# Kernel optimization log

Measured on AMD Instinct MI355X. Metric: run time of the kernel, lower is better.

The kernel has to match this reference:

```python
import jax, jax.numpy as jnp
import numpy as np

B, T, C = 2, 2048, 1024
H = 16
D = C // H
STRIDE = 2
EPS = 1e-5


def _strided_allowed(T, stride):
    # position i attends to j if j<=i and (j >= i-4 local band OR j % stride == 0)
    i = jnp.arange(T)[:, None]
    j = jnp.arange(T)[None, :]
    return (j <= i) & ((j >= i - 4) | (j % stride == 0))


def _layernorm(x, w, b):
    mu = jnp.mean(x, axis=-1, keepdims=True)
    var = jnp.mean(jnp.square(x - mu), axis=-1, keepdims=True)
    return (x - mu) * jax.lax.rsqrt(var + EPS) * w + b


def setup_inputs() -> dict:
    key = jax.random.key(0)
    ks = jax.random.split(key, 8)
    s = 0.02
    return {
        "x": jax.random.normal(ks[0], (B, T, C), dtype=jnp.float32),
        "ln1_w": jnp.ones((C,), jnp.float32),
        "ln1_b": jnp.zeros((C,), jnp.float32),
        "c_attn_w": s * jax.random.normal(ks[1], (C, 3 * C), jnp.float32),  # [in,out]
        "c_attn_b": jnp.zeros((3 * C,), jnp.float32),
        "attn_proj_w": s * jax.random.normal(ks[2], (C, C), jnp.float32),
        "attn_proj_b": jnp.zeros((C,), jnp.float32),
        "ln2_w": jnp.ones((C,), jnp.float32),
        "ln2_b": jnp.zeros((C,), jnp.float32),
        "fc_w": s * jax.random.normal(ks[3], (C, 4 * C), jnp.float32),
        "fc_b": jnp.zeros((4 * C,), jnp.float32),
        "mlp_proj_w": s * jax.random.normal(ks[4], (4 * C, C), jnp.float32),
        "mlp_proj_b": jnp.zeros((C,), jnp.float32),
    }


def reference(x, ln1_w, ln1_b, c_attn_w, c_attn_b, attn_proj_w, attn_proj_b,
              ln2_w, ln2_b, fc_w, fc_b, mlp_proj_w, mlp_proj_b):
    Bx, Tx, Cx = x.shape
    # --- sparse (strided) causal attention on ln_1(x) ---
    h = _layernorm(x, ln1_w, ln1_b)
    qkv = h @ c_attn_w + c_attn_b                      # [B,T,3C]
    q, k, v = jnp.split(qkv, 3, axis=-1)
    q = q.reshape(Bx, Tx, H, D).transpose(0, 2, 1, 3)  # [B,H,T,D]
    k = k.reshape(Bx, Tx, H, D).transpose(0, 2, 1, 3)
    v = v.reshape(Bx, Tx, H, D).transpose(0, 2, 1, 3)
    scale = 1.0 / np.sqrt(D)
    att = jnp.einsum('bhqd,bhkd->bhqk', q, k) * scale  # dense [B,H,T,T] as in source
    allowed = _strided_allowed(Tx, STRIDE)             # [T,T] bool
    att = jnp.where(allowed[None, None], att, -jnp.inf)
    att = jax.nn.softmax(att, axis=-1)
    y = jnp.einsum('bhqk,bhkd->bhqd', att, v)
    y = y.transpose(0, 2, 1, 3).reshape(Bx, Tx, Cx)
    y = y @ attn_proj_w + attn_proj_b
    x = x + y
    # --- MLP on ln_2(x) ---
    h2 = _layernorm(x, ln2_w, ln2_b)
    h2 = jax.nn.gelu(h2 @ fc_w + fc_b, approximate=False)
    x = x + (h2 @ mlp_proj_w + mlp_proj_b)
    return x
```

## Files before the change

### kernel.cpp

```cpp
#include <hip/hip_runtime.h>
#include <hip/hip_bf16.h>

#define Bn 2
#define Tn 2048
#define Cn 1024
#define Hn 16
#define Dn 64
#define Mrows (Bn * Tn)

typedef __attribute__((ext_vector_type(8))) short short8;
typedef __attribute__((ext_vector_type(4))) float f32x4;

typedef const __attribute__((address_space(1))) unsigned int* gas_ptr;
typedef __attribute__((address_space(3))) unsigned int* las_ptr;

__device__ __forceinline__ unsigned short f2b(float f) {
  unsigned int u = __builtin_bit_cast(unsigned int, f);
  return (unsigned short)((u + 0x7fffu + ((u >> 16) & 1u)) >> 16);
}

__device__ __forceinline__ float gelu_f(float v) {
  float u2 = v + 0.044715f * v * v * v;
  float e = __expf(1.5957691216f * u2);
  float th = 1.0f - 2.0f / (e + 1.0f);
  return 0.5f * v * (1.0f + th);
}

__device__ __forceinline__ void ln_row(const float* __restrict__ x, const float* __restrict__ w,
                                       const float* __restrict__ b, unsigned short* __restrict__ out,
                                       int row, float* ls, float* ls2) {
  const int t = threadIdx.x;
  const float4 v = *reinterpret_cast<const float4*>(x + (size_t)row * Cn + t * 4);
  float s = v.x + v.y + v.z + v.w;
  float s2 = v.x * v.x + v.y * v.y + v.z * v.z + v.w * v.w;
#pragma unroll
  for (int m = 1; m < 64; m <<= 1) { s += __shfl_xor(s, m); s2 += __shfl_xor(s2, m); }
  if ((t & 63) == 0) { ls[t >> 6] = s; ls2[t >> 6] = s2; }
  __syncthreads();
  s  = ls[0] + ls[1] + ls[2] + ls[3];
  s2 = ls2[0] + ls2[1] + ls2[2] + ls2[3];
  const float mu = s * (1.0f / Cn);
  const float rstd = rsqrtf(s2 * (1.0f / Cn) - mu * mu + 1e-5f);
  const float4 wv = *reinterpret_cast<const float4*>(w + t * 4);
  const float4 bv = *reinterpret_cast<const float4*>(b + t * 4);
  unsigned short o[4];
  o[0] = f2b((v.x - mu) * rstd * wv.x + bv.x);
  o[1] = f2b((v.y - mu) * rstd * wv.y + bv.y);
  o[2] = f2b((v.z - mu) * rstd * wv.z + bv.z);
  o[3] = f2b((v.w - mu) * rstd * wv.w + bv.w);
  *reinterpret_cast<uint2*>(out + (size_t)row * Cn + t * 4) = *reinterpret_cast<uint2*>(o);
}

__global__ __launch_bounds__(256) void ln_kernel(const float* __restrict__ x,
                                                 const float* __restrict__ w,
                                                 const float* __restrict__ b,
                                                 unsigned short* __restrict__ out) {
  __shared__ float ls[4], ls2[4];
  ln_row(x, w, b, out, blockIdx.x, ls, ls2);
}

__global__ __launch_bounds__(256) void prep_kernel(
    const float* __restrict__ W0, unsigned short* __restrict__ T0,
    const float* __restrict__ W1, unsigned short* __restrict__ T1,
    const float* __restrict__ W2, unsigned short* __restrict__ T2,
    const float* __restrict__ W3, unsigned short* __restrict__ T3,
    const float* __restrict__ x, const float* __restrict__ ln1w,
    const float* __restrict__ ln1b, unsigned short* __restrict__ h) {
  __shared__ float tile[32][33];
  __shared__ float ls[4], ls2[4];
  int b = blockIdx.x;
  if (b >= 12288) {
    ln_row(x, ln1w, ln1b, h, b - 12288, ls, ls2);
    return;
  }
  const float* W; unsigned short* T; int K, N;
  if (b < 3072)      { W = W0; T = T0; K = 1024; N = 3072; }
  else if (b < 4096) { W = W1; T = T1; K = 1024; N = 1024; b -= 3072; }
  else if (b < 8192) { W = W2; T = T2; K = 1024; N = 4096; b -= 4096; }
  else               { W = W3; T = T3; K = 4096; N = 1024; b -= 8192; }
  const int nx = N >> 5;
  const int n0 = (b % nx) * 32, k0 = (b / nx) * 32;
  const int tx = threadIdx.x & 31, ty = threadIdx.x >> 5;
#pragma unroll
  for (int r = 0; r < 4; r++)
    tile[ty + r * 8][tx] = W[(size_t)(k0 + ty + r * 8) * N + n0 + tx];
  __syncthreads();
#pragma unroll
  for (int r = 0; r < 4; r++)
    T[(size_t)(n0 + ty + r * 8) * K + k0 + tx] = f2b(tile[tx][ty + r * 8]);
}

#define BUFS 16384
template <int EP>
__global__ __launch_bounds__(512, 2) void gemm256_kernel(
    const unsigned short* __restrict__ A, const unsigned short* __restrict__ Bt,
    const float* __restrict__ bias, void* out, int M, int N, int K, int nx) {
  extern __shared__ unsigned short lds[];
  const int tid = threadIdx.x;
  const int lane = tid & 63, w = tid >> 6;
  const int wm = w >> 2, wn = w & 3;
  const int l15 = lane & 15, l4 = lane >> 4;

  const int nwg = gridDim.x;
  int wg = blockIdx.x;
  wg = (wg & 7) * (nwg >> 3) + (wg >> 3);
  const int tile_m = (wg / nx) * 256;
  const int tile_n = (wg % nx) * 256;

  f32x4 acc[8][4] = {};

  const int ch0 = w * 64 + lane;
  const int r0 = ch0 >> 2;
  const int c0 = (((ch0 & 3) ^ ((r0 >> 1) & 3))) * 8;
  const unsigned short* gA0 = A + (size_t)(tile_m + r0) * K + c0;
  const unsigned short* gA1 = gA0 + (size_t)128 * K;
  const unsigned short* gB0 = Bt + (size_t)(tile_n + r0) * K + c0;
  const unsigned short* gB1 = gB0 + (size_t)128 * K;
  const int ldsA0 = (w * 64) * 8, ldsA1 = (512 + w * 64) * 8;

  auto stage = [&](unsigned short* Ab, int t) {
    unsigned short* Bb = Ab + 8192;
    const size_t ko = (size_t)t * 32;
    __builtin_amdgcn_global_load_lds((gas_ptr)(gA0 + ko), (las_ptr)&Ab[ldsA0], 16, 0, 0);
    __builtin_amdgcn_global_load_lds((gas_ptr)(gA1 + ko), (las_ptr)&Ab[ldsA1], 16, 0, 0);
    __builtin_amdgcn_global_load_lds((gas_ptr)(gB0 + ko), (las_ptr)&Bb[ldsA0], 16, 0, 0);
    __builtin_amdgcn_global_load_lds((gas_ptr)(gB1 + ko), (las_ptr)&Bb[ldsA1], 16, 0, 0);
  };

  stage(lds, 0);
  stage(lds + BUFS, 1);
  stage(lds + 2 * BUFS, 2);
  asm volatile("s_waitcnt vmcnt(8)" ::: "memory");
  __builtin_amdgcn_s_barrier();
  __builtin_amdgcn_sched_barrier(0);

  const int ca = (l4 ^ ((l15 >> 1) & 3)) * 8;

  const int nt = K >> 5;
  for (int tb = 0; tb < nt; tb += 4) {
#pragma unroll
    for (int u = 0; u < 4; u++) {
      const int t = tb + u;
      if (t + 3 < nt) stage(lds + (((u + 3) & 3) * BUFS), t + 3);

      const unsigned short* Ab = lds + u * BUFS;
      const unsigned short* Bb = Ab + 8192;
      short8 a[4], b[4], a2[4];
#pragma unroll
      for (int i = 0; i < 4; i++) {
        a[i] = *reinterpret_cast<const short8*>(&Ab[(wm * 128 + i * 16 + l15) * 32 + ca]);
        b[i] = *reinterpret_cast<const short8*>(&Bb[(wn * 64 + i * 16 + l15) * 32 + ca]);
      }
      __builtin_amdgcn_sched_barrier(0);
#pragma unroll
      for (int i = 0; i < 4; i++)
        a2[i] = *reinterpret_cast<const short8*>(&Ab[(wm * 128 + 64 + i * 16 + l15) * 32 + ca]);

      asm volatile("s_waitcnt lgkmcnt(4)" ::: "memory");
      __builtin_amdgcn_sched_barrier(0);
      __builtin_amdgcn_s_setprio(1);
#pragma unroll
      for (int mi = 0; mi < 4; mi++)
#pragma unroll
        for (int ni = 0; ni < 4; ni++)
          acc[mi][ni] = __builtin_amdgcn_mfma_f32_16x16x32_bf16(a[mi], b[ni], acc[mi][ni], 0, 0, 0);
      __builtin_amdgcn_s_setprio(0);
      __builtin_amdgcn_sched_barrier(0);

      asm volatile("s_waitcnt lgkmcnt(0)" ::: "memory");
      __builtin_amdgcn_sched_barrier(0);
      __builtin_amdgcn_s_setprio(1);
#pragma unroll
      for (int mi = 0; mi < 4; mi++)
#pragma unroll
        for (int ni = 0; ni < 4; ni++)
          acc[mi + 4][ni] = __builtin_amdgcn_mfma_f32_16x16x32_bf16(a2[mi], b[ni], acc[mi + 4][ni], 0, 0, 0);
      __builtin_amdgcn_s_setprio(0);
      __builtin_amdgcn_sched_barrier(0);

      if (t + 3 < nt) {
        asm volatile("s_waitcnt vmcnt(8)" ::: "memory");
      } else if (t + 2 < nt) {
        asm volatile("s_waitcnt vmcnt(4)" ::: "memory");
      } else if (t + 1 < nt) {
        asm volatile("s_waitcnt vmcnt(0)" ::: "memory");
      }
      __builtin_amdgcn_s_barrier();
      __builtin_amdgcn_sched_barrier(0);
    }
  }

#pragma unroll
  for (int ni = 0; ni < 4; ni++) {
    const int col = tile_n + wn * 64 + ni * 16 + l15;
    const float bv = bias[col];
#pragma unroll
    for (int mi = 0; mi < 8; mi++) {
#pragma unroll
      for (int r = 0; r < 4; r++) {
        const int row = tile_m + wm * 128 + mi * 16 + l4 * 4 + r;
        const size_t idx = (size_t)row * N + col;
        float v = acc[mi][ni][r] + bv;
        if (EP == 0) {
          ((unsigned short*)out)[idx] = f2b(v);
        } else {
          ((unsigned short*)out)[idx] = f2b(gelu_f(v));
        }
      }
    }
  }
}

__global__ __launch_bounds__(512, 1) void gemm128_kernel(
    const unsigned short* __restrict__ A, const unsigned short* __restrict__ Bt,
    const float* __restrict__ bias, const float* __restrict__ res, float* __restrict__ out,
    int M, int N, int K, int nx) {
  extern __shared__ unsigned short lds[];
  const int tid = threadIdx.x;
  const int lane = tid & 63, w = tid >> 6;
  const int wm = w >> 2, wn = w & 3;
  const int l15 = lane & 15, l4 = lane >> 4;

  const int nwg = gridDim.x;
  int wg = blockIdx.x;
  wg = (wg & 7) * (nwg >> 3) + (wg >> 3);
  const int tile_m = (wg / nx) * 128;
  const int tile_n = (wg % nx) * 128;

  f32x4 acc[4][2] = {};

  const unsigned short* Gs = (w < 4) ? A : Bt;
  const int tb0 = (w < 4) ? tile_m : tile_n;
  const int ch0 = (w & 3) * 128 + lane;
  const int r0c = ch0 >> 2;
  const int c0s = (((ch0 & 3) ^ ((r0c >> 1) & 3))) * 8;
  const unsigned short* g0 = Gs + (size_t)(tb0 + r0c) * K + c0s;
  const unsigned short* g1 = g0 + (size_t)16 * K;
  const int lds0 = ((w & 3) * 128) * 8, lds1 = ((w & 3) * 128 + 64) * 8;
  const int half = (w < 4) ? 0 : 4096;

  auto stage = [&](int slot, int t) {
    unsigned short* Lb = lds + slot * 8192 + half;
    const size_t ko = (size_t)t * 32;
    __builtin_amdgcn_global_load_lds((gas_ptr)(g0 + ko), (las_ptr)&Lb[lds0], 16, 0, 0);
    __builtin_amdgcn_global_load_lds((gas_ptr)(g1 + ko), (las_ptr)&Lb[lds1], 16, 0, 0);
  };

  stage(0, 0);
  stage(1, 1);
  stage(2, 2);
  stage(3, 3);
  asm volatile("s_waitcnt vmcnt(4)" ::: "memory");
  __builtin_amdgcn_s_barrier();
  __builtin_amdgcn_sched_barrier(0);

  const int ca = (l4 ^ ((l15 >> 1) & 3)) * 8;

  const int nt = K >> 5;
  const int np = nt >> 1;
  for (int p = 0; p < np; ++p) {
    const int t0 = 2 * p;
    if (t0 + 4 < nt) stage((t0 + 4) % 6, t0 + 4);
    if (t0 + 5 < nt) stage((t0 + 5) % 6, t0 + 5);

    const unsigned short* A0 = lds + (t0 % 6) * 8192;
    const unsigned short* B0 = A0 + 4096;
    const unsigned short* A1 = lds + ((t0 + 1) % 6) * 8192;
    const unsigned short* B1 = A1 + 4096;
    short8 a[2], b[2], a2[2], c[2], d[2], c2[2];
#pragma unroll
    for (int i = 0; i < 2; i++) {
      a[i] = *reinterpret_cast<const short8*>(&A0[(wm * 64 + i * 16 + l15) * 32 + ca]);
      b[i] = *reinterpret_cast<const short8*>(&B0[(wn * 32 + i * 16 + l15) * 32 + ca]);
    }
    __builtin_amdgcn_sched_barrier(0);
#pragma unroll
    for (int i = 0; i < 2; i++)
      a2[i] = *reinterpret_cast<const short8*>(&A0[(wm * 64 + 32 + i * 16 + l15) * 32 + ca]);
    __builtin_amdgcn_sched_barrier(0);
#pragma unroll
    for (int i = 0; i < 2; i++) {
      c[i] = *reinterpret_cast<const short8*>(&A1[(wm * 64 + i * 16 + l15) * 32 + ca]);
      d[i] = *reinterpret_cast<const short8*>(&B1[(wn * 32 + i * 16 + l15) * 32 + ca]);
    }
    __builtin_amdgcn_sched_barrier(0);
#pragma unroll
    for (int i = 0; i < 2; i++)
      c2[i] = *reinterpret_cast<const short8*>(&A1[(wm * 64 + 32 + i * 16 + l15) * 32 + ca]);

    asm volatile("s_waitcnt lgkmcnt(8)" ::: "memory");
    __builtin_amdgcn_sched_barrier(0);
    __builtin_amdgcn_s_setprio(1);
#pragma unroll
    for (int mi = 0; mi < 2; mi++)
#pragma unroll
      for (int ni = 0; ni < 2; ni++)
        acc[mi][ni] = __builtin_amdgcn_mfma_f32_16x16x32_bf16(a[mi], b[ni], acc[mi][ni], 0, 0, 0);
    __builtin_amdgcn_s_setprio(0);
    __builtin_amdgcn_sched_barrier(0);

    asm volatile("s_waitcnt lgkmcnt(6)" ::: "memory");
    __builtin_amdgcn_sched_barrier(0);
    __builtin_amdgcn_s_setprio(1);
#pragma unroll
    for (int mi = 0; mi < 2; mi++)
#pragma unroll
      for (int ni = 0; ni < 2; ni++)
        acc[mi + 2][ni] = __builtin_amdgcn_mfma_f32_16x16x32_bf16(a2[mi], b[ni], acc[mi + 2][ni], 0, 0, 0);
    __builtin_amdgcn_s_setprio(0);
    __builtin_amdgcn_sched_barrier(0);

    asm volatile("s_waitcnt lgkmcnt(2)" ::: "memory");
    __builtin_amdgcn_sched_barrier(0);
    __builtin_amdgcn_s_setprio(1);
#pragma unroll
    for (int mi = 0; mi < 2; mi++)
#pragma unroll
      for (int ni = 0; ni < 2; ni++)
        acc[mi][ni] = __builtin_amdgcn_mfma_f32_16x16x32_bf16(c[mi], d[ni], acc[mi][ni], 0, 0, 0);
    __builtin_amdgcn_s_setprio(0);
    __builtin_amdgcn_sched_barrier(0);

    asm volatile("s_waitcnt lgkmcnt(0)" ::: "memory");
    __builtin_amdgcn_sched_barrier(0);
    __builtin_amdgcn_s_setprio(1);
#pragma unroll
    for (int mi = 0; mi < 2; mi++)
#pragma unroll
      for (int ni = 0; ni < 2; ni++)
        acc[mi + 2][ni] = __builtin_amdgcn_mfma_f32_16x16x32_bf16(c2[mi], d[ni], acc[mi + 2][ni], 0, 0, 0);
    __builtin_amdgcn_s_setprio(0);
    __builtin_amdgcn_sched_barrier(0);

    if (t0 + 4 < nt) {
      asm volatile("s_waitcnt vmcnt(4)" ::: "memory");
    } else if (t0 + 2 < nt) {
      asm volatile("s_waitcnt vmcnt(0)" ::: "memory");
    }
    __builtin_amdgcn_s_barrier();
    __builtin_amdgcn_sched_barrier(0);
  }

#pragma unroll
  for (int ni = 0; ni < 2; ni++) {
    const int col = tile_n + wn * 32 + ni * 16 + l15;
    const float bv = bias[col];
#pragma unroll
    for (int mi = 0; mi < 4; mi++) {
#pragma unroll
      for (int r = 0; r < 4; r++) {
        const int row = tile_m + wm * 64 + mi * 16 + l4 * 4 + r;
        const size_t idx = (size_t)row * N + col;
        out[idx] = acc[mi][ni][r] + bv + res[idx];
      }
    }
  }
}

__global__ __launch_bounds__(256, 4) void attn_kernel(const unsigned short* __restrict__ qkv,
                                                      unsigned short* __restrict__ y) {
  __shared__ unsigned short SH[17408];
  const int tid = threadIdx.x;
  const int lane = tid & 63, w = tid >> 6;
  const int l15 = lane & 15, l4 = lane >> 4;

  const int bi = blockIdx.x;
  const int quarter = bi >> 8, rest = bi & 255;
  const int bh = rest >> 3, sub = rest & 7;
  int qt;
  if (quarter == 0) qt = sub;
  else if (quarter == 1) qt = 15 - sub;
  else if (quarter == 2) qt = 16 + sub;
  else qt = 31 - sub;
  const int bb = bh >> 4, hh = bh & 15;
  const int q0 = qt * 64;
  const size_t base = (size_t)bb * Tn * (3 * Cn) + hh * 64;

  const int nfar = qt >> 1;
  const int ntiles = nfar + (q0 ? 2 : 1);

  unsigned short* Vt = SH + 8192;
  unsigned short* Ps = SH + 12800 + w * 1152;

  auto keyof = [&](int t, int row) -> int {
    if (t < nfar) return t * 128 + 2 * row;
    return q0 - 64 * (ntiles - 1 - t) + row;
  };
  auto stageK = [&](int t) {
    unsigned short* kb = SH + ((t & 1) << 12);
#pragma unroll
    for (int u = 0; u < 2; u++) {
      const int chunk = u * 256 + tid;
      const int row = chunk >> 3, cc = chunk & 7;
      const int csrc = cc ^ (row & 7);
      const int key = keyof(t, row);
      __builtin_amdgcn_global_load_lds(
          (gas_ptr)&qkv[base + Cn + (size_t)key * (3 * Cn) + csrc * 8],
          (las_ptr)&kb[(u * 256 + (w << 6)) * 8], 16, 0, 0);
    }
  };
  uint4 vr[2];
  auto fetchV = [&](int t) {
#pragma unroll
    for (int u = 0; u < 2; u++) {
      const int chunk = u * 256 + tid;
      const int row = chunk >> 3, cc = chunk & 7;
      const int key = keyof(t, row);
      vr[u] = *reinterpret_cast<const uint4*>(&qkv[base + 2 * Cn + (size_t)key * (3 * Cn) + cc * 8]);
    }
  };

#pragma unroll
  for (int u = 0; u < 2; u++) {
    const int chunk = u * 256 + tid;
    const int row = chunk >> 3, cc = chunk & 7;
    const int csrc = cc ^ (row & 7);
    __builtin_amdgcn_global_load_lds(
        (gas_ptr)&qkv[base + (size_t)(q0 + row) * (3 * Cn) + csrc * 8],
        (las_ptr)&SH[(u * 256 + (w << 6)) * 8], 16, 0, 0);
  }
  __syncthreads();
  short8 qf[2];
#pragma unroll
  for (int ks = 0; ks < 2; ks++) {
    const int r = (w << 4) + l15;
    qf[ks] = *reinterpret_cast<const short8*>(&SH[r * 64 + (((ks * 4 + l4) ^ (l15 & 7)) * 8)]);
  }
  asm volatile("s_waitcnt lgkmcnt(0)" ::: "memory");
  __builtin_amdgcn_s_barrier();
  __builtin_amdgcn_sched_barrier(0);
  stageK(0);
  fetchV(0);
  __syncthreads();

  f32x4 acc_o[4] = {};
  float mrow[4], lrow[4];
#pragma unroll
  for (int r = 0; r < 4; r++) { mrow[r] = -1e30f; lrow[r] = 0.0f; }

  for (int t = 0; t < ntiles; ++t) {
#pragma unroll
    for (int u = 0; u < 2; u++) {
      const int chunk = u * 256 + tid;
      const int row = chunk >> 3, cc = chunk & 7;
      unsigned short tmp[8];
      *reinterpret_cast<uint4*>(tmp) = vr[u];
      const int xr = row ^ (cc << 3);
#pragma unroll
      for (int j = 0; j < 8; j++) Vt[(cc * 8 + j) * 72 + xr] = tmp[j];
    }
    if (t + 1 < ntiles) { stageK(t + 1); fetchV(t + 1); }
    asm volatile("s_waitcnt lgkmcnt(0)" ::: "memory");
    __builtin_amdgcn_s_barrier();
    __builtin_amdgcn_sched_barrier(0);

    const unsigned short* Kb = SH + ((t & 1) << 12);
    f32x4 s[4] = {};
#pragma unroll
    for (int ni = 0; ni < 4; ni++) {
#pragma unroll
      for (int ks = 0; ks < 2; ks++) {
        const int r = ni * 16 + l15;
        short8 kf = *reinterpret_cast<const short8*>(&Kb[r * 64 + (((ks * 4 + l4) ^ (l15 & 7)) * 8)]);
        s[ni] = __builtin_amdgcn_mfma_f32_16x16x32_bf16(qf[ks], kf, s[ni], 0, 0, 0);
      }
    }

    const bool far = (t < nfar);
    const int kb0 = far ? t * 128 : q0 - 64 * (ntiles - 1 - t);
#pragma unroll
    for (int ni = 0; ni < 4; ni++) {
      const int pos = ni * 16 + l15;
      const int j = far ? kb0 + 2 * pos : kb0 + pos;
#pragma unroll
      for (int r = 0; r < 4; r++) {
        float v = s[ni][r] * 0.125f;
        if (far) {
          v = (j < q0 - 64) ? v : -1e30f;
        } else {
          const int iq = q0 + (w << 4) + l4 * 4 + r;
          const bool ok = (j <= iq) && ((j >= iq - 4) || ((j & 1) == 0));
          v = ok ? v : -1e30f;
        }
        s[ni][r] = v;
      }
    }

    float tmx[4];
    bool need = false;
#pragma unroll
    for (int r = 0; r < 4; r++) {
      float tm = fmaxf(fmaxf(s[0][r], s[1][r]), fmaxf(s[2][r], s[3][r]));
      tm = fmaxf(tm, __shfl_xor(tm, 1));
      tm = fmaxf(tm, __shfl_xor(tm, 2));
      tm = fmaxf(tm, __shfl_xor(tm, 4));
      tm = fmaxf(tm, __shfl_xor(tm, 8));
      tmx[r] = tm;
      need = need || (tm > mrow[r] + 8.0f);
    }
    if (__any(need)) {
#pragma unroll
      for (int r = 0; r < 4; r++) {
        const float mnew = fmaxf(mrow[r], tmx[r]);
        const float alpha = __expf(mrow[r] - mnew);
        mrow[r] = mnew;
        lrow[r] *= alpha;
#pragma unroll
        for (int nd = 0; nd < 4; nd++) acc_o[nd][r] *= alpha;
      }
    }
#pragma unroll
    for (int r = 0; r < 4; r++) {
      float rs = 0.0f;
#pragma unroll
      for (int ni = 0; ni < 4; ni++) {
        const float pv = __expf(s[ni][r] - mrow[r]);
        s[ni][r] = pv;
        rs += pv;
      }
      rs += __shfl_xor(rs, 1); rs += __shfl_xor(rs, 2);
      rs += __shfl_xor(rs, 4); rs += __shfl_xor(rs, 8);
      lrow[r] += rs;
    }

#pragma unroll
    for (int ni = 0; ni < 4; ni++)
#pragma unroll
      for (int r = 0; r < 4; r++)
        Ps[(l4 * 4 + r) * 72 + ni * 16 + l15] = f2b(s[ni][r]);

#pragma unroll
    for (int kss = 0; kss < 2; kss++) {
      short8 pf = *reinterpret_cast<const short8*>(&Ps[l15 * 72 + kss * 32 + l4 * 8]);
#pragma unroll
      for (int nd = 0; nd < 4; nd++) {
        const int d = nd * 16 + l15;
        const int kcol = (kss * 32 + l4 * 8) ^ ((d >> 3) << 3);
        short8 vf = *reinterpret_cast<const short8*>(&Vt[d * 72 + kcol]);
        acc_o[nd] = __builtin_amdgcn_mfma_f32_16x16x32_bf16(pf, vf, acc_o[nd], 0, 0, 0);
      }
    }

    __syncthreads();
  }

#pragma unroll
  for (int r = 0; r < 4; r++) {
    const float inv = 1.0f / lrow[r];
    const int row = q0 + (w << 4) + l4 * 4 + r;
#pragma unroll
    for (int nd = 0; nd < 4; nd++) {
      const int col = nd * 16 + l15;
      y[((size_t)bb * Tn + row) * Cn + hh * 64 + col] = f2b(acc_o[nd][r] * inv);
    }
  }
}

extern "C" void kernel_launch(void* const* d_in, const int* in_sizes, int n_in,
                              void* d_out, int out_size, void* d_ws, size_t ws_size,
                              hipStream_t stream) {
  const float* x           = (const float*)d_in[0];
  const float* ln1_w       = (const float*)d_in[1];
  const float* ln1_b       = (const float*)d_in[2];
  const float* c_attn_w    = (const float*)d_in[3];
  const float* c_attn_b    = (const float*)d_in[4];
  const float* attn_proj_w = (const float*)d_in[5];
  const float* attn_proj_b = (const float*)d_in[6];
  const float* ln2_w       = (const float*)d_in[7];
  const float* ln2_b       = (const float*)d_in[8];
  const float* fc_w        = (const float*)d_in[9];
  const float* fc_b        = (const float*)d_in[10];
  const float* mlp_proj_w  = (const float*)d_in[11];
  const float* mlp_proj_b  = (const float*)d_in[12];
  float* out = (float*)d_out;

  char* ws = (char*)d_ws;
  unsigned short* wT1 = (unsigned short*)(ws);
  unsigned short* wT2 = (unsigned short*)(ws + 6291456);
  unsigned short* wT3 = (unsigned short*)(ws + 8388608);
  unsigned short* wT4 = (unsigned short*)(ws + 16777216);
  unsigned short* h   = (unsigned short*)(ws + 25165824);
  unsigned short* qkv = (unsigned short*)(ws + 33554432);
  unsigned short* yb  = (unsigned short*)(ws + 67108864);

  hipFuncSetAttribute((const void*)gemm256_kernel<0>, hipFuncAttributeMaxDynamicSharedMemorySize, 131072);
  hipFuncSetAttribute((const void*)gemm256_kernel<2>, hipFuncAttributeMaxDynamicSharedMemorySize, 131072);
  hipFuncSetAttribute((const void*)gemm128_kernel, hipFuncAttributeMaxDynamicSharedMemorySize, 98304);

  prep_kernel<<<16384, 256, 0, stream>>>(c_attn_w, wT1, attn_proj_w, wT2,
                                         fc_w, wT3, mlp_proj_w, wT4,
                                         x, ln1_w, ln1_b, h);
  gemm256_kernel<0><<<(Mrows / 256) * (3072 / 256), 512, 131072, stream>>>(
      h, wT1, c_attn_b, qkv, Mrows, 3072, 1024, 3072 / 256);
  attn_kernel<<<1024, 256, 0, stream>>>(qkv, yb);
  gemm128_kernel<<<(Mrows / 128) * (1024 / 128), 512, 98304, stream>>>(
      yb, wT2, attn_proj_b, x, out, Mrows, 1024, 1024, 1024 / 128);
  ln_kernel<<<Mrows, 256, 0, stream>>>(out, ln2_w, ln2_b, h);
  gemm256_kernel<2><<<(Mrows / 256) * (4096 / 256), 512, 131072, stream>>>(
      h, wT3, fc_b, qkv, Mrows, 4096, 1024, 4096 / 256);
  gemm128_kernel<<<(Mrows / 128) * (1024 / 128), 512, 98304, stream>>>(
      qkv, wT4, mlp_proj_b, out, out, Mrows, 1024, 4096, 1024 / 128);
}
```

Baseline: 221.4 us.

## Retile QKV GEMM to 256x192, use 128-tile GEMM for FC, pipeline attention loads

The QKV projection GEMM moves from 256x256 to 256x192 tiles, with A and B loads split across waves, so the 3072-wide output produces 256 workgroups instead of 192 and fills the CUs better. The FC GEMM switches to the 128x128 kernel, which gains a GELU bf16 epilogue, giving more workgroups. The attention kernel reorders its V/K prefetch and replaces full syncthreads with partial vmcnt waits so global loads overlap compute. The risks are lower per-tile data reuse, lower occupancy from launch_bounds(512,1), and wait counts that must match exactly.

```diff
diff --git a/kernel.cpp b/kernel.cpp
--- a/kernel.cpp
+++ b/kernel.cpp
@@ -90,9 +90,8 @@
     T[(size_t)(n0 + ty + r * 8) * K + k0 + tx] = f2b(tile[tx][ty + r * 8]);
 }
 
-#define BUFS 16384
 template <int EP>
-__global__ __launch_bounds__(512, 2) void gemm256_kernel(
+__global__ __launch_bounds__(512, 1) void gemm192_kernel(
     const unsigned short* __restrict__ A, const unsigned short* __restrict__ Bt,
     const float* __restrict__ bias, void* out, int M, int N, int K, int nx) {
   extern __shared__ unsigned short lds[];
@@ -105,32 +104,36 @@
   int wg = blockIdx.x;
   wg = (wg & 7) * (nwg >> 3) + (wg >> 3);
   const int tile_m = (wg / nx) * 256;
-  const int tile_n = (wg % nx) * 256;
-
-  f32x4 acc[8][4] = {};
-
-  const int ch0 = w * 64 + lane;
+  const int tile_n = (wg % nx) * 192;
+
+  f32x4 acc[8][3] = {};
+
+  const bool isA = (w < 4);
+  const int wl = w & 3;
+  const int ch0 = wl * 64 + lane;
   const int r0 = ch0 >> 2;
   const int c0 = (((ch0 & 3) ^ ((r0 >> 1) & 3))) * 8;
-  const unsigned short* gA0 = A + (size_t)(tile_m + r0) * K + c0;
-  const unsigned short* gA1 = gA0 + (size_t)128 * K;
-  const unsigned short* gB0 = Bt + (size_t)(tile_n + r0) * K + c0;
-  const unsigned short* gB1 = gB0 + (size_t)128 * K;
-  const int ldsA0 = (w * 64) * 8, ldsA1 = (512 + w * 64) * 8;
-
-  auto stage = [&](unsigned short* Ab, int t) {
-    unsigned short* Bb = Ab + 8192;
+  const unsigned short* G = isA ? A : Bt;
+  const int tb0 = isA ? tile_m : tile_n;
+  const unsigned short* g0 = G + (size_t)(tb0 + r0) * K + c0;
+  const int lb = wl * 512;
+
+  auto stage = [&](int slot, int t) {
+    unsigned short* L = lds + slot * 14336 + (isA ? 0 : 8192);
     const size_t ko = (size_t)t * 32;
-    __builtin_amdgcn_global_load_lds((gas_ptr)(gA0 + ko), (las_ptr)&Ab[ldsA0], 16, 0, 0);
-    __builtin_amdgcn_global_load_lds((gas_ptr)(gA1 + ko), (las_ptr)&Ab[ldsA1], 16, 0, 0);
-    __builtin_amdgcn_global_load_lds((gas_ptr)(gB0 + ko), (las_ptr)&Bb[ldsA0], 16, 0, 0);
-    __builtin_amdgcn_global_load_lds((gas_ptr)(gB1 + ko), (las_ptr)&Bb[ldsA1], 16, 0, 0);
+#pragma unroll
+    for (int j = 0; j < 4; j++) {
+      if (isA || j < 3)
+        __builtin_amdgcn_global_load_lds((gas_ptr)(g0 + (size_t)64 * K * j + ko),
+                                         (las_ptr)&L[lb + j * 2048], 16, 0, 0);
+    }
   };
 
-  stage(lds, 0);
-  stage(lds + BUFS, 1);
-  stage(lds + 2 * BUFS, 2);
-  asm volatile("s_waitcnt vmcnt(8)" ::: "memory");
+  stage(0, 0);
+  stage(1, 1);
+  stage(2, 2);
+  if (isA) asm volatile("s_waitcnt vmcnt(8)" ::: "memory");
+  else     asm volatile("s_waitcnt vmcnt(6)" ::: "memory");
   __builtin_amdgcn_s_barrier();
   __builtin_amdgcn_sched_barrier(0);
 
@@ -141,16 +144,17 @@
 #pragma unroll
     for (int u = 0; u < 4; u++) {
       const int t = tb + u;
-      if (t + 3 < nt) stage(lds + (((u + 3) & 3) * BUFS), t + 3);
-
-      const unsigned short* Ab = lds + u * BUFS;
+      if (t + 3 < nt) stage((u + 3) & 3, t + 3);
+
+      const unsigned short* Ab = lds + u * 14336;
       const unsigned short* Bb = Ab + 8192;
-      short8 a[4], b[4], a2[4];
-#pragma unroll
-      for (int i = 0; i < 4; i++) {
+      short8 a[4], b[3], a2[4];
+#pragma unroll
+      for (int i = 0; i < 4; i++)
         a[i] = *reinterpret_cast<const short8*>(&Ab[(wm * 128 + i * 16 + l15) * 32 + ca]);
-        b[i] = *reinterpret_cast<const short8*>(&Bb[(wn * 64 + i * 16 + l15) * 32 + ca]);
-      }
+#pragma unroll
+      for (int i = 0; i < 3; i++)
+        b[i] = *reinterpret_cast<const short8*>(&Bb[(wn * 48 + i * 16 + l15) * 32 + ca]);
       __builtin_amdgcn_sched_barrier(0);
 #pragma unroll
       for (int i = 0; i < 4; i++)
@@ -162,7 +166,7 @@
 #pragma unroll
       for (int mi = 0; mi < 4; mi++)
 #pragma unroll
-        for (int ni = 0; ni < 4; ni++)
+        for (int ni = 0; ni < 3; ni++)
           acc[mi][ni] = __builtin_amdgcn_mfma_f32_16x16x32_bf16(a[mi], b[ni], acc[mi][ni], 0, 0, 0);
       __builtin_amdgcn_s_setprio(0);
       __builtin_amdgcn_sched_barrier(0);
@@ -173,15 +177,17 @@
 #pragma unroll
       for (int mi = 0; mi < 4; mi++)
 #pragma unroll
-        for (int ni = 0; ni < 4; ni++)
+        for (int ni = 0; ni < 3; ni++)
           acc[mi + 4][ni] = __builtin_amdgcn_mfma_f32_16x16x32_bf16(a2[mi], b[ni], acc[mi + 4][ni], 0, 0, 0);
       __builtin_amdgcn_s_setprio(0);
       __builtin_amdgcn_sched_barrier(0);
 
       if (t + 3 < nt) {
-        asm volatile("s_waitcnt vmcnt(8)" ::: "memory");
+        if (isA) asm volatile("s_waitcnt vmcnt(8)" ::: "memory");
+        else     asm volatile("s_waitcnt vmcnt(6)" ::: "memory");
       } else if (t + 2 < nt) {
-        asm volatile("s_waitcnt vmcnt(4)" ::: "memory");
+        if (isA) asm volatile("s_waitcnt vmcnt(4)" ::: "memory");
+        else     asm volatile("s_waitcnt vmcnt(3)" ::: "memory");
       } else if (t + 1 < nt) {
         asm volatile("s_waitcnt vmcnt(0)" ::: "memory");
       }
@@ -191,8 +197,8 @@
   }
 
 #pragma unroll
-  for (int ni = 0; ni < 4; ni++) {
-    const int col = tile_n + wn * 64 + ni * 16 + l15;
+  for (int ni = 0; ni < 3; ni++) {
+    const int col = tile_n + wn * 48 + ni * 16 + l15;
     const float bv = bias[col];
 #pragma unroll
     for (int mi = 0; mi < 8; mi++) {
@@ -211,9 +217,10 @@
   }
 }
 
+template <int EP>
 __global__ __launch_bounds__(512, 1) void gemm128_kernel(
     const unsigned short* __restrict__ A, const unsigned short* __restrict__ Bt,
-    const float* __restrict__ bias, const float* __restrict__ res, float* __restrict__ out,
+    const float* __restrict__ bias, const float* __restrict__ res, void* __restrict__ outv,
     int M, int N, int K, int nx) {
   extern __shared__ unsigned short lds[];
   const int tid = threadIdx.x;
@@ -351,7 +358,12 @@
       for (int r = 0; r < 4; r++) {
         const int row = tile_m + wm * 64 + mi * 16 + l4 * 4 + r;
         const size_t idx = (size_t)row * N + col;
-        out[idx] = acc[mi][ni][r] + bv + res[idx];
+        float v = acc[mi][ni][r] + bv;
+        if (EP == 1) {
+          ((float*)outv)[idx] = v + res[idx];
+        } else {
+          ((unsigned short*)outv)[idx] = f2b(gelu_f(v));
+        }
       }
     }
   }
@@ -449,8 +461,13 @@
 #pragma unroll
       for (int j = 0; j < 8; j++) Vt[(cc * 8 + j) * 72 + xr] = tmp[j];
     }
-    if (t + 1 < ntiles) { stageK(t + 1); fetchV(t + 1); }
-    asm volatile("s_waitcnt lgkmcnt(0)" ::: "memory");
+    if (t + 1 < ntiles) { fetchV(t + 1); stageK(t + 1); }
+    __builtin_amdgcn_sched_barrier(0);
+    if (t + 1 < ntiles) {
+      asm volatile("s_waitcnt vmcnt(4) lgkmcnt(0)" ::: "memory");
+    } else {
+      asm volatile("s_waitcnt vmcnt(0) lgkmcnt(0)" ::: "memory");
+    }
     __builtin_amdgcn_s_barrier();
     __builtin_amdgcn_sched_barrier(0);
 
@@ -541,7 +558,13 @@
       }
     }
 
-    __syncthreads();
+    if (t + 1 < ntiles) {
+      asm volatile("s_waitcnt vmcnt(2) lgkmcnt(0)" ::: "memory");
+    } else {
+      asm volatile("s_waitcnt lgkmcnt(0)" ::: "memory");
+    }
+    __builtin_amdgcn_s_barrier();
+    __builtin_amdgcn_sched_barrier(0);
   }
 
 #pragma unroll
@@ -583,21 +606,21 @@
   unsigned short* qkv = (unsigned short*)(ws + 33554432);
   unsigned short* yb  = (unsigned short*)(ws + 67108864);
 
-  hipFuncSetAttribute((const void*)gemm256_kernel<0>, hipFuncAttributeMaxDynamicSharedMemorySize, 131072);
-  hipFuncSetAttribute((const void*)gemm256_kernel<2>, hipFuncAttributeMaxDynamicSharedMemorySize, 131072);
-  hipFuncSetAttribute((const void*)gemm128_kernel, hipFuncAttributeMaxDynamicSharedMemorySize, 98304);
+  hipFuncSetAttribute((const void*)gemm192_kernel<0>, hipFuncAttributeMaxDynamicSharedMemorySize, 114688);
+  hipFuncSetAttribute((const void*)gemm128_kernel<1>, hipFuncAttributeMaxDynamicSharedMemorySize, 98304);
+  hipFuncSetAttribute((const void*)gemm128_kernel<2>, hipFuncAttributeMaxDynamicSharedMemorySize, 98304);
 
   prep_kernel<<<16384, 256, 0, stream>>>(c_attn_w, wT1, attn_proj_w, wT2,
                                          fc_w, wT3, mlp_proj_w, wT4,
                                          x, ln1_w, ln1_b, h);
-  gemm256_kernel<0><<<(Mrows / 256) * (3072 / 256), 512, 131072, stream>>>(
-      h, wT1, c_attn_b, qkv, Mrows, 3072, 1024, 3072 / 256);
+  gemm192_kernel<0><<<(Mrows / 256) * (3072 / 192), 512, 114688, stream>>>(
+      h, wT1, c_attn_b, qkv, Mrows, 3072, 1024, 3072 / 192);
   attn_kernel<<<1024, 256, 0, stream>>>(qkv, yb);
-  gemm128_kernel<<<(Mrows / 128) * (1024 / 128), 512, 98304, stream>>>(
+  gemm128_kernel<1><<<(Mrows / 128) * (1024 / 128), 512, 98304, stream>>>(
       yb, wT2, attn_proj_b, x, out, Mrows, 1024, 1024, 1024 / 128);
   ln_kernel<<<Mrows, 256, 0, stream>>>(out, ln2_w, ln2_b, h);
-  gemm256_kernel<2><<<(Mrows / 256) * (4096 / 256), 512, 131072, stream>>>(
-      h, wT3, fc_b, qkv, Mrows, 4096, 1024, 4096 / 256);
-  gemm128_kernel<<<(Mrows / 128) * (1024 / 128), 512, 98304, stream>>>(
+  gemm128_kernel<2><<<(Mrows / 128) * (4096 / 128), 512, 98304, stream>>>(
+      h, wT3, fc_b, nullptr, qkv, Mrows, 4096, 1024, 4096 / 128);
+  gemm128_kernel<1><<<(Mrows / 128) * (1024 / 128), 512, 98304, stream>>>(
       qkv, wT4, mlp_proj_b, out, out, Mrows, 1024, 4096, 1024 / 128);
 }
```

After: 231.7 us. 4.6% more time.
